# Optimization experiments

Measured on AMD Instinct MI355X. Metric: run time of the kernel, lower is better.

## Reference

```python
import jax, jax.numpy as jnp
import numpy as np

IMG_SIZE = 1280
STRIDE = 4
NUM_CLASSES = 80
TOPK = 1000
NMS_THRESH = 0.6
SCALE_CLAMP = float(np.log(1000.0))  # DEFAULT_SCALE_CLAMP
N_ANCHORS = (IMG_SIZE // STRIDE) ** 2  # 102400


def _anchors():
    # generate_anchors: meshgrid over fmp, stacked as (x, y), flattened
    fmp = IMG_SIZE // STRIDE
    ys, xs = jnp.meshgrid(jnp.arange(fmp), jnp.arange(fmp), indexing='ij')
    return jnp.stack([xs, ys], axis=-1).reshape(-1, 2).astype(jnp.float32)


def _decode_boxes(anchors, reg):
    # [wl, ht, wr, hb] -> [x1, y1, x2, y2], scaled by stride
    reg = jnp.exp(jnp.minimum(reg, SCALE_CLAMP))
    xy1 = anchors - reg[..., :2]
    xy2 = anchors + reg[..., 2:]
    return jnp.concatenate([xy1, xy2], axis=-1) * STRIDE


def _iou_matrix(b):
    # pairwise IoU with the exact eps handling of the original numpy NMS
    x1, y1, x2, y2 = b[:, 0], b[:, 1], b[:, 2], b[:, 3]
    areas = (x2 - x1) * (y2 - y1)
    xx1 = jnp.maximum(x1[:, None], x1[None, :])
    yy1 = jnp.maximum(y1[:, None], y1[None, :])
    xx2 = jnp.minimum(x2[:, None], x2[None, :])
    yy2 = jnp.minimum(y2[:, None], y2[None, :])
    w = jnp.maximum(1e-10, xx2 - xx1)
    h = jnp.maximum(1e-10, yy2 - yy1)
    inter = w * h
    return inter / (areas[:, None] + areas[None, :] - inter + 1e-10)


def _greedy_nms(iou, same_class):
    # boxes are pre-sorted by score descending (top_k output order), so a
    # single greedy pass with a same-class mask is equivalent to the
    # original per-class loop (each class subset preserves score order).
    K = iou.shape[0]
    suppress = (iou > NMS_THRESH) & same_class
    idx = jnp.arange(K)

    def body(keep, i):
        row = suppress[i] & keep[i]  # only a kept box suppresses others
        keep = keep & ~(row & (idx > i))
        return keep, None

    keep0 = jnp.ones((K,), dtype=bool)
    keep, _ = jax.lax.scan(body, keep0, idx)
    return keep


def setup_inputs() -> dict:
    key = jax.random.key(0)
    k1, k2, k3 = jax.random.split(key, 3)
    hmp_pred = jax.random.normal(k1, (N_ANCHORS, NUM_CLASSES), dtype=jnp.float32)
    reg_pred = jax.random.normal(k2, (N_ANCHORS, 4), dtype=jnp.float32)
    iou_pred = jax.random.normal(k3, (N_ANCHORS, 1), dtype=jnp.float32)
    return {"hmp_pred": hmp_pred, "reg_pred": reg_pred, "iou_pred": iou_pred}


def reference(hmp_pred, reg_pred, iou_pred):
    # score fusion: sqrt(sigmoid(hmp) * sigmoid(iou)), max over classes
    fused = jnp.sqrt(jax.nn.sigmoid(hmp_pred) * jax.nn.sigmoid(iou_pred))  # [N, C]
    scores = jnp.max(fused, axis=-1)
    labels = jnp.argmax(fused, axis=-1)

    # top-k selection (sorted descending)
    scores, indices = jax.lax.top_k(scores, TOPK)
    labels = labels[indices]
    reg = reg_pred[indices]
    anc = _anchors()[indices]

    # decode + normalize + clamp
    bboxes = jnp.clip(_decode_boxes(anc, reg) / IMG_SIZE, 0.0, 1.0)  # [K, 4]

    # class-aware greedy NMS; keep mask replaces the dynamic-shape filter
    same_class = labels[:, None] == labels[None, :]
    keep = _greedy_nms(_iou_matrix(bboxes), same_class)
    return scores, labels, bboxes, keep
```

## Files before the change

kernel.cpp:

```cpp
#include <hip/hip_runtime.h>
#include <stdint.h>

#define N_ANCH 102400
#define FMP 320
#define K_TOP 1000
#define NMS_T 0.6f
#define SC_CLAMP 6.907755278982137f
#define IMGF 1280.0f
#define NBINS 16384

#define OFF_SCORES   0u
#define OFF_LABELS   409600u
#define OFF_META     884736u
#define OFF_KEYS     884992u
#define OFF_BOXES    917760u
#define OFF_LAB1K    933760u
#define OFF_MASK     937760u
#define OFF_DIAG     1065760u

__device__ __forceinline__ float sigf(float x) {
    return 1.0f / (1.0f + expf(-x));
}

__global__ __launch_bounds__(256) void k_scores(const float* __restrict__ hmp,
                                                const float* __restrict__ iou,
                                                float* __restrict__ scores,
                                                uint32_t* __restrict__ labels,
                                                uint64_t* __restrict__ diag) {
    int blk = blockIdx.x;
    if (blk == 0) {
#pragma unroll
        for (int k = 0; k < 4; ++k) diag[threadIdx.x * 4 + k] = 0ull;
    }
    int gid = blk * 256 + threadIdx.x;
    int a = gid >> 2;
    int q = gid & 3;
    float si = sigf(iou[a]);
    const float4* row4 = (const float4*)hmp + (size_t)a * 20 + q;
    float4 v[5];
#pragma unroll
    for (int j = 0; j < 5; ++j) v[j] = row4[j * 4];
    float best = -1.0f;
    int bc = 0;
#pragma unroll
    for (int j = 0; j < 5; ++j) {
        int cb = j * 16 + q * 4;
        float f;
        f = sqrtf(sigf(v[j].x) * si); if (f > best) { best = f; bc = cb; }
        f = sqrtf(sigf(v[j].y) * si); if (f > best) { best = f; bc = cb + 1; }
        f = sqrtf(sigf(v[j].z) * si); if (f > best) { best = f; bc = cb + 2; }
        f = sqrtf(sigf(v[j].w) * si); if (f > best) { best = f; bc = cb + 3; }
    }
#pragma unroll
    for (int off = 1; off <= 2; off <<= 1) {
        float of = __shfl_xor(best, off);
        int   oc = __shfl_xor(bc, off);
        if (of > best || (of == best && oc < bc)) { best = of; bc = oc; }
    }
    if (q == 0) {
        scores[a] = best;
        labels[a] = (uint32_t)bc;
    }
}

__global__ __launch_bounds__(1024) void k_histcollect(const float* __restrict__ scores,
                                                      uint32_t* __restrict__ meta,
                                                      uint64_t* __restrict__ keys) {
    __shared__ uint32_t lh[NBINS];
    __shared__ uint32_t coarse[1024];
    __shared__ uint32_t s_cut, ccnt;

    const int tid = threadIdx.x;
    for (int i = tid; i < NBINS; i += 1024) lh[i] = 0u;
    if (tid == 0) { ccnt = 0u; s_cut = 0u; }
    __syncthreads();

    const float4* s4 = (const float4*)scores;
    for (int k = tid; k < N_ANCH / 4; k += 1024) {
        float4 v = s4[k];
        atomicAdd(&lh[__float_as_uint(v.x) >> 16], 1u);
        atomicAdd(&lh[__float_as_uint(v.y) >> 16], 1u);
        atomicAdd(&lh[__float_as_uint(v.z) >> 16], 1u);
        atomicAdd(&lh[__float_as_uint(v.w) >> 16], 1u);
    }
    __syncthreads();

    {
        uint32_t s = 0;
#pragma unroll
        for (int b = 0; b < 16; ++b) s += lh[tid * 16 + b];
        coarse[tid] = s;
    }
    __syncthreads();
    for (int off = 1; off < 1024; off <<= 1) {
        uint32_t v = coarse[tid] + ((tid + off < 1024) ? coarse[tid + off] : 0u);
        __syncthreads();
        coarse[tid] = v;
        __syncthreads();
    }
    {
        uint32_t inc   = coarse[tid];
        uint32_t above = (tid < 1023) ? coarse[tid + 1] : 0u;
        if (above < K_TOP && inc >= K_TOP) {
            uint32_t cnt = above;
            for (int b = 15; b >= 0; --b) {
                cnt += lh[tid * 16 + b];
                if (cnt >= K_TOP) { s_cut = (uint32_t)(tid * 16 + b); break; }
            }
        }
    }
    __syncthreads();

    const uint32_t cut = s_cut;
    for (int k = tid; k < N_ANCH / 4; k += 1024) {
        float4 v = s4[k];
        uint32_t bb[4] = { __float_as_uint(v.x), __float_as_uint(v.y),
                           __float_as_uint(v.z), __float_as_uint(v.w) };
#pragma unroll
        for (int c = 0; c < 4; ++c) {
            if ((bb[c] >> 16) >= cut) {
                uint32_t p = atomicAdd(&ccnt, 1u);
                if (p < 4096u)
                    keys[p] = ((uint64_t)bb[c] << 32) |
                              (uint64_t)(0xFFFFFFFFu - (uint32_t)(k * 4 + c));
            }
        }
    }
    __syncthreads();
    if (tid == 0) meta[2] = ccnt;
}

__global__ __launch_bounds__(1024) void k_rank(const uint64_t* __restrict__ keys,
                                               const uint32_t* __restrict__ meta,
                                               const uint32_t* __restrict__ labels,
                                               const float* __restrict__ reg,
                                               float* __restrict__ out,
                                               float* __restrict__ boxes,
                                               uint32_t* __restrict__ lab1k) {
    __shared__ uint64_t sk[4096];
    uint32_t M = meta[2];
    if (M > 4096u) M = 4096u;
    if ((uint32_t)(blockIdx.x * 16) >= M) return;
    for (uint32_t i = threadIdx.x; i < M; i += 1024) sk[i] = keys[i];
    __syncthreads();
    int lane = threadIdx.x & 63;
    int wg = blockIdx.x * 16 + (threadIdx.x >> 6);
    if ((uint32_t)wg >= M) return;
    uint64_t mykey = sk[wg];
    uint32_t rank = 0;
    for (uint32_t j = lane; j < M; j += 64) rank += (sk[j] > mykey) ? 1u : 0u;
#pragma unroll
    for (int off = 32; off; off >>= 1) rank += __shfl_xor(rank, off);
    if (lane != 0 || rank >= K_TOP) return;
    int t = (int)rank;
    uint32_t sbits = (uint32_t)(mykey >> 32);
    uint32_t idx   = 0xFFFFFFFFu - (uint32_t)(mykey & 0xFFFFFFFFull);
    float score = __uint_as_float(sbits);
    uint32_t lab = labels[idx];
    out[t]         = score;
    out[K_TOP + t] = (float)lab;
    lab1k[t]       = lab;
    float ax = (float)(idx % FMP);
    float ay = (float)(idx / FMP);
    float4 rr = ((const float4*)reg)[idx];
    float e0 = expf(fminf(rr.x, SC_CLAMP));
    float e1 = expf(fminf(rr.y, SC_CLAMP));
    float e2 = expf(fminf(rr.z, SC_CLAMP));
    float e3 = expf(fminf(rr.w, SC_CLAMP));
    float x1 = fminf(fmaxf((ax - e0) * 4.0f / IMGF, 0.0f), 1.0f);
    float y1 = fminf(fmaxf((ay - e1) * 4.0f / IMGF, 0.0f), 1.0f);
    float x2 = fminf(fmaxf((ax + e2) * 4.0f / IMGF, 0.0f), 1.0f);
    float y2 = fminf(fmaxf((ay + e3) * 4.0f / IMGF, 0.0f), 1.0f);
    out[2 * K_TOP + t * 4 + 0] = x1;
    out[2 * K_TOP + t * 4 + 1] = y1;
    out[2 * K_TOP + t * 4 + 2] = x2;
    out[2 * K_TOP + t * 4 + 3] = y2;
    boxes[t * 4 + 0] = x1;
    boxes[t * 4 + 1] = y1;
    boxes[t * 4 + 2] = x2;
    boxes[t * 4 + 3] = y2;
}

__global__ __launch_bounds__(1024) void k_mask(const float* __restrict__ boxes,
                                               const uint32_t* __restrict__ lab1k,
                                               uint64_t* __restrict__ mask,
                                               uint64_t* __restrict__ diag) {
    int r = blockIdx.x * 16 + (threadIdx.x >> 6);
    int lane = threadIdx.x & 63;
    if (r >= K_TOP) return;
    float4 bi = ((const float4*)boxes)[r];
    uint32_t li = lab1k[r];
    float areai = (bi.z - bi.x) * (bi.w - bi.y);
    int iw = r >> 6;
    uint64_t dw = 0ull;
#pragma unroll
    for (int w = 0; w < 16; ++w) {
        int j = w * 64 + lane;
        bool sup = false;
        if (j < K_TOP && j > r) {
            float4 bj = ((const float4*)boxes)[j];
            float areaj = (bj.z - bj.x) * (bj.w - bj.y);
            float xx1 = fmaxf(bi.x, bj.x);
            float yy1 = fmaxf(bi.y, bj.y);
            float xx2 = fminf(bi.z, bj.z);
            float yy2 = fminf(bi.w, bj.w);
            float ww = fmaxf(1e-10f, xx2 - xx1);
            float hh = fmaxf(1e-10f, yy2 - yy1);
            float inter = ww * hh;
            float iouv = inter / (areai + areaj - inter + 1e-10f);
            sup = (iouv > NMS_T) && (li == lab1k[j]);
        }
        unsigned long long m = __ballot(sup);
        if (lane == 0) mask[(size_t)r * 16 + w] = (uint64_t)m;
        if (w == iw) dw = (uint64_t)m;
    }
    if (lane == 0) diag[r] = dw;
}

__global__ __launch_bounds__(64, 1) void k_scan(const uint64_t* __restrict__ mask,
                                                const uint64_t* __restrict__ diag,
                                                float* __restrict__ out) {
    int lane = threadIdx.x;
    int q = lane >> 4, wrd = lane & 15;
    uint64_t remv = 0ull;
    uint64_t dcur = diag[lane];
    for (int g = 0; g < 16; ++g) {
        uint64_t dnxt = (g < 15) ? diag[64 * (g + 1) + lane] : 0ull;
        uint64_t bun[16];
        if (g < 15) {
#pragma unroll
            for (int r4 = 0; r4 < 16; ++r4)
                bun[r4] = mask[(size_t)(64 * g + 4 * r4 + q) * 16 + wrd];
        }
        uint32_t dlo = 0, dhi = 0;
#pragma unroll
        for (int qq = 0; qq < 4; ++qq) {
            dlo |= __builtin_amdgcn_readlane((uint32_t)remv, qq * 16 + g);
            dhi |= __builtin_amdgcn_readlane((uint32_t)(remv >> 32), qq * 16 + g);
        }
        uint64_t D = ((uint64_t)dhi << 32) | dlo;
#pragma unroll
        for (int b = 0; b < 64; ++b) {
            uint32_t tlo = __builtin_amdgcn_readlane((uint32_t)dcur, b);
            uint32_t thi = __builtin_amdgcn_readlane((uint32_t)(dcur >> 32), b);
            uint64_t T = ((uint64_t)thi << 32) | tlo;
            uint64_t sel = ((D >> b) & 1ull) - 1ull;
            D |= T & sel;
        }
        uint64_t keepg = ~D;
        int j = g * 64 + lane;
        if (j < K_TOP) out[6 * K_TOP + j] = (float)((keepg >> lane) & 1ull);
        if (g < 15) {
#pragma unroll
            for (int r4 = 0; r4 < 16; ++r4) {
                uint32_t kb = (uint32_t)(keepg >> (4 * r4 + q)) & 1u;
                uint64_t mm = 0ull - (uint64_t)kb;
                remv |= bun[r4] & mm;
            }
        }
        dcur = dnxt;
    }
}

extern "C" void kernel_launch(void* const* d_in, const int* in_sizes, int n_in,
                              void* d_out, int out_size, void* d_ws, size_t ws_size,
                              hipStream_t stream) {
    const float* hmp = (const float*)d_in[0];
    const float* reg = (const float*)d_in[1];
    const float* iou = (const float*)d_in[2];
    float* out = (float*)d_out;
    char* ws = (char*)d_ws;

    float*    scores = (float*)(ws + OFF_SCORES);
    uint32_t* labels = (uint32_t*)(ws + OFF_LABELS);
    uint32_t* meta   = (uint32_t*)(ws + OFF_META);
    uint64_t* keys   = (uint64_t*)(ws + OFF_KEYS);
    float*    boxes  = (float*)(ws + OFF_BOXES);
    uint32_t* lab1k  = (uint32_t*)(ws + OFF_LAB1K);
    uint64_t* mask   = (uint64_t*)(ws + OFF_MASK);
    uint64_t* diag   = (uint64_t*)(ws + OFF_DIAG);

    k_scores<<<dim3(N_ANCH * 4 / 256), dim3(256), 0, stream>>>(hmp, iou, scores, labels, diag);
    k_histcollect<<<dim3(1), dim3(1024), 0, stream>>>(scores, meta, keys);
    k_rank<<<dim3(256), dim3(1024), 0, stream>>>(keys, meta, labels, reg, out, boxes, lab1k);
    k_mask<<<dim3(63), dim3(1024), 0, stream>>>(boxes, lab1k, mask, diag);
    k_scan<<<dim3(1), dim3(64), 0, stream>>>(mask, diag, out);
}
```

Before: 148.6 us.

## Fuse histogram collect and rank into single kernel with bucketed rank

```diff
diff --git a/kernel.cpp b/kernel.cpp
--- a/kernel.cpp
+++ b/kernel.cpp
@@ -11,8 +11,6 @@
 
 #define OFF_SCORES   0u
 #define OFF_LABELS   409600u
-#define OFF_META     884736u
-#define OFF_KEYS     884992u
 #define OFF_BOXES    917760u
 #define OFF_LAB1K    933760u
 #define OFF_MASK     937760u
@@ -63,16 +61,24 @@
     }
 }
 
-__global__ __launch_bounds__(1024) void k_histcollect(const float* __restrict__ scores,
-                                                      uint32_t* __restrict__ meta,
-                                                      uint64_t* __restrict__ keys) {
+__global__ __launch_bounds__(1024) void k_topk(const float* __restrict__ scores,
+                                               const uint32_t* __restrict__ labels,
+                                               const float* __restrict__ reg,
+                                               float* __restrict__ out,
+                                               float* __restrict__ boxes,
+                                               uint32_t* __restrict__ lab1k) {
     __shared__ uint32_t lh[NBINS];
-    __shared__ uint32_t coarse[1024];
-    __shared__ uint32_t s_cut, ccnt;
+    __shared__ uint32_t coarse[1025];
+    __shared__ uint64_t skey[4096];
+    __shared__ uint32_t cnt[2048];
+    __shared__ uint16_t sst[4096];
+    __shared__ uint16_t sen[4096];
+    __shared__ uint32_t s_cut, s_m;
 
     const int tid = threadIdx.x;
     for (int i = tid; i < NBINS; i += 1024) lh[i] = 0u;
-    if (tid == 0) { ccnt = 0u; s_cut = 0u; }
+    for (int i = tid; i < 2048; i += 1024) cnt[i] = 0u;
+    if (tid == 0) { s_cut = 0u; coarse[1024] = 0u; }
     __syncthreads();
 
     const float4* s4 = (const float4*)scores;
@@ -102,83 +108,85 @@
         uint32_t inc   = coarse[tid];
         uint32_t above = (tid < 1023) ? coarse[tid + 1] : 0u;
         if (above < K_TOP && inc >= K_TOP) {
-            uint32_t cnt = above;
+            uint32_t c2 = above;
             for (int b = 15; b >= 0; --b) {
-                cnt += lh[tid * 16 + b];
-                if (cnt >= K_TOP) { s_cut = (uint32_t)(tid * 16 + b); break; }
+                c2 += lh[tid * 16 + b];
+                if (c2 >= K_TOP) { s_cut = (uint32_t)(tid * 16 + b); break; }
             }
         }
     }
     __syncthreads();
-
     const uint32_t cut = s_cut;
+    if (tid == 0) {
+        uint32_t tc = cut >> 4;
+        uint32_t m = coarse[tc + 1];
+        for (uint32_t k2 = cut; k2 < tc * 16 + 16; ++k2) m += lh[k2];
+        s_m = (m > 4096u) ? 4096u : m;
+    }
+
     for (int k = tid; k < N_ANCH / 4; k += 1024) {
         float4 v = s4[k];
         uint32_t bb[4] = { __float_as_uint(v.x), __float_as_uint(v.y),
                            __float_as_uint(v.z), __float_as_uint(v.w) };
 #pragma unroll
         for (int c = 0; c < 4; ++c) {
-            if ((bb[c] >> 16) >= cut) {
-                uint32_t p = atomicAdd(&ccnt, 1u);
-                if (p < 4096u)
-                    keys[p] = ((uint64_t)bb[c] << 32) |
-                              (uint64_t)(0xFFFFFFFFu - (uint32_t)(k * 4 + c));
+            uint32_t b = bb[c] >> 16;
+            if (b >= cut) {
+                uint32_t tb = b >> 4;
+                uint32_t base = coarse[tb + 1];
+                for (uint32_t k2 = b + 1; k2 < tb * 16 + 16; ++k2) base += lh[k2];
+                uint32_t sp = b - cut;
+                if (sp < 2048u) {
+                    uint32_t slot = atomicAdd(&cnt[sp], 1u);
+                    uint32_t pos  = base + slot;
+                    uint32_t end  = base + lh[b];
+                    if (pos < 4096u) {
+                        skey[pos] = ((uint64_t)bb[c] << 32) |
+                                    (uint64_t)(0xFFFFFFFFu - (uint32_t)(k * 4 + c));
+                        sst[pos] = (uint16_t)base;
+                        sen[pos] = (uint16_t)((end > 4096u) ? 4096u : end);
+                    }
+                }
             }
         }
     }
     __syncthreads();
-    if (tid == 0) meta[2] = ccnt;
-}
-
-__global__ __launch_bounds__(1024) void k_rank(const uint64_t* __restrict__ keys,
-                                               const uint32_t* __restrict__ meta,
-                                               const uint32_t* __restrict__ labels,
-                                               const float* __restrict__ reg,
-                                               float* __restrict__ out,
-                                               float* __restrict__ boxes,
-                                               uint32_t* __restrict__ lab1k) {
-    __shared__ uint64_t sk[4096];
-    uint32_t M = meta[2];
-    if (M > 4096u) M = 4096u;
-    if ((uint32_t)(blockIdx.x * 16) >= M) return;
-    for (uint32_t i = threadIdx.x; i < M; i += 1024) sk[i] = keys[i];
-    __syncthreads();
-    int lane = threadIdx.x & 63;
-    int wg = blockIdx.x * 16 + (threadIdx.x >> 6);
-    if ((uint32_t)wg >= M) return;
-    uint64_t mykey = sk[wg];
-    uint32_t rank = 0;
-    for (uint32_t j = lane; j < M; j += 64) rank += (sk[j] > mykey) ? 1u : 0u;
-#pragma unroll
-    for (int off = 32; off; off >>= 1) rank += __shfl_xor(rank, off);
-    if (lane != 0 || rank >= K_TOP) return;
-    int t = (int)rank;
-    uint32_t sbits = (uint32_t)(mykey >> 32);
-    uint32_t idx   = 0xFFFFFFFFu - (uint32_t)(mykey & 0xFFFFFFFFull);
-    float score = __uint_as_float(sbits);
-    uint32_t lab = labels[idx];
-    out[t]         = score;
-    out[K_TOP + t] = (float)lab;
-    lab1k[t]       = lab;
-    float ax = (float)(idx % FMP);
-    float ay = (float)(idx / FMP);
-    float4 rr = ((const float4*)reg)[idx];
-    float e0 = expf(fminf(rr.x, SC_CLAMP));
-    float e1 = expf(fminf(rr.y, SC_CLAMP));
-    float e2 = expf(fminf(rr.z, SC_CLAMP));
-    float e3 = expf(fminf(rr.w, SC_CLAMP));
-    float x1 = fminf(fmaxf((ax - e0) * 4.0f / IMGF, 0.0f), 1.0f);
-    float y1 = fminf(fmaxf((ay - e1) * 4.0f / IMGF, 0.0f), 1.0f);
-    float x2 = fminf(fmaxf((ax + e2) * 4.0f / IMGF, 0.0f), 1.0f);
-    float y2 = fminf(fmaxf((ay + e3) * 4.0f / IMGF, 0.0f), 1.0f);
-    out[2 * K_TOP + t * 4 + 0] = x1;
-    out[2 * K_TOP + t * 4 + 1] = y1;
-    out[2 * K_TOP + t * 4 + 2] = x2;
-    out[2 * K_TOP + t * 4 + 3] = y2;
-    boxes[t * 4 + 0] = x1;
-    boxes[t * 4 + 1] = y1;
-    boxes[t * 4 + 2] = x2;
-    boxes[t * 4 + 3] = y2;
+
+    const uint32_t M = s_m;
+    for (uint32_t s2 = tid; s2 < M; s2 += 1024) {
+        uint64_t key = skey[s2];
+        uint32_t st = sst[s2], en = sen[s2];
+        uint32_t r = st;
+        for (uint32_t u = st; u < en; ++u) r += (skey[u] > key) ? 1u : 0u;
+        if (r >= K_TOP) continue;
+        int t = (int)r;
+        uint32_t sbits = (uint32_t)(key >> 32);
+        uint32_t idx   = 0xFFFFFFFFu - (uint32_t)(key & 0xFFFFFFFFull);
+        float score = __uint_as_float(sbits);
+        uint32_t lab = labels[idx];
+        out[t]         = score;
+        out[K_TOP + t] = (float)lab;
+        lab1k[t]       = lab;
+        float ax = (float)(idx % FMP);
+        float ay = (float)(idx / FMP);
+        float4 rr = ((const float4*)reg)[idx];
+        float e0 = expf(fminf(rr.x, SC_CLAMP));
+        float e1 = expf(fminf(rr.y, SC_CLAMP));
+        float e2 = expf(fminf(rr.z, SC_CLAMP));
+        float e3 = expf(fminf(rr.w, SC_CLAMP));
+        float x1 = fminf(fmaxf((ax - e0) * 4.0f / IMGF, 0.0f), 1.0f);
+        float y1 = fminf(fmaxf((ay - e1) * 4.0f / IMGF, 0.0f), 1.0f);
+        float x2 = fminf(fmaxf((ax + e2) * 4.0f / IMGF, 0.0f), 1.0f);
+        float y2 = fminf(fmaxf((ay + e3) * 4.0f / IMGF, 0.0f), 1.0f);
+        out[2 * K_TOP + t * 4 + 0] = x1;
+        out[2 * K_TOP + t * 4 + 1] = y1;
+        out[2 * K_TOP + t * 4 + 2] = x2;
+        out[2 * K_TOP + t * 4 + 3] = y2;
+        boxes[t * 4 + 0] = x1;
+        boxes[t * 4 + 1] = y1;
+        boxes[t * 4 + 2] = x2;
+        boxes[t * 4 + 3] = y2;
+    }
 }
 
 __global__ __launch_bounds__(1024) void k_mask(const float* __restrict__ boxes,
@@ -273,16 +281,13 @@
 
     float*    scores = (float*)(ws + OFF_SCORES);
     uint32_t* labels = (uint32_t*)(ws + OFF_LABELS);
-    uint32_t* meta   = (uint32_t*)(ws + OFF_META);
-    uint64_t* keys   = (uint64_t*)(ws + OFF_KEYS);
     float*    boxes  = (float*)(ws + OFF_BOXES);
     uint32_t* lab1k  = (uint32_t*)(ws + OFF_LAB1K);
     uint64_t* mask   = (uint64_t*)(ws + OFF_MASK);
     uint64_t* diag   = (uint64_t*)(ws + OFF_DIAG);
 
     k_scores<<<dim3(N_ANCH * 4 / 256), dim3(256), 0, stream>>>(hmp, iou, scores, labels, diag);
-    k_histcollect<<<dim3(1), dim3(1024), 0, stream>>>(scores, meta, keys);
-    k_rank<<<dim3(256), dim3(1024), 0, stream>>>(keys, meta, labels, reg, out, boxes, lab1k);
+    k_topk<<<dim3(1), dim3(1024), 0, stream>>>(scores, labels, reg, out, boxes, lab1k);
     k_mask<<<dim3(63), dim3(1024), 0, stream>>>(boxes, lab1k, mask, diag);
     k_scan<<<dim3(1), dim3(64), 0, stream>>>(mask, diag, out);
 }
```

Result: slower. 178.2 us (+19.9%).

## Split single-block histogram/collect into multi-block hist and cut-collect kernels

Applied to the files above, without the earlier changes.

```diff
diff --git a/kernel.cpp b/kernel.cpp
--- a/kernel.cpp
+++ b/kernel.cpp
@@ -11,6 +11,7 @@
 
 #define OFF_SCORES   0u
 #define OFF_LABELS   409600u
+#define OFF_HIST     819200u
 #define OFF_META     884736u
 #define OFF_KEYS     884992u
 #define OFF_BOXES    917760u
@@ -26,9 +27,14 @@
                                                 const float* __restrict__ iou,
                                                 float* __restrict__ scores,
                                                 uint32_t* __restrict__ labels,
+                                                uint32_t* __restrict__ hist,
+                                                uint32_t* __restrict__ meta,
                                                 uint64_t* __restrict__ diag) {
     int blk = blockIdx.x;
-    if (blk == 0) {
+    if (blk < 64) {
+        hist[blk * 256 + threadIdx.x] = 0u;
+    } else if (blk == 64) {
+        if (threadIdx.x < 64) meta[threadIdx.x] = 0u;
 #pragma unroll
         for (int k = 0; k < 4; ++k) diag[threadIdx.x * 4 + k] = 0ull;
     }
@@ -63,26 +69,35 @@
     }
 }
 
-__global__ __launch_bounds__(1024) void k_histcollect(const float* __restrict__ scores,
-                                                      uint32_t* __restrict__ meta,
-                                                      uint64_t* __restrict__ keys) {
+__global__ __launch_bounds__(1024) void k_hist(const float* __restrict__ scores,
+                                               uint32_t* __restrict__ hist) {
+    __shared__ uint32_t lh[NBINS];
+    const int tid = threadIdx.x;
+    for (int i = tid; i < NBINS; i += 1024) lh[i] = 0u;
+    __syncthreads();
+    int base = blockIdx.x * 3200;
+    for (int k = tid; k < 3200; k += 1024) {
+        uint32_t bin = __float_as_uint(scores[base + k]) >> 16;
+        atomicAdd(&lh[bin], 1u);
+    }
+    __syncthreads();
+    for (int i = tid; i < NBINS; i += 1024) {
+        uint32_t c = lh[i];
+        if (c) atomicAdd(&hist[i], c);
+    }
+}
+
+__global__ __launch_bounds__(1024) void k_cutcollect(const float* __restrict__ scores,
+                                                     const uint32_t* __restrict__ hist,
+                                                     uint32_t* __restrict__ meta,
+                                                     uint64_t* __restrict__ keys) {
     __shared__ uint32_t lh[NBINS];
     __shared__ uint32_t coarse[1024];
-    __shared__ uint32_t s_cut, ccnt;
+    __shared__ uint32_t s_cut, cnt, cbase;
 
     const int tid = threadIdx.x;
-    for (int i = tid; i < NBINS; i += 1024) lh[i] = 0u;
-    if (tid == 0) { ccnt = 0u; s_cut = 0u; }
-    __syncthreads();
-
-    const float4* s4 = (const float4*)scores;
-    for (int k = tid; k < N_ANCH / 4; k += 1024) {
-        float4 v = s4[k];
-        atomicAdd(&lh[__float_as_uint(v.x) >> 16], 1u);
-        atomicAdd(&lh[__float_as_uint(v.y) >> 16], 1u);
-        atomicAdd(&lh[__float_as_uint(v.z) >> 16], 1u);
-        atomicAdd(&lh[__float_as_uint(v.w) >> 16], 1u);
-    }
+    for (int i = tid; i < NBINS; i += 1024) lh[i] = hist[i];
+    if (tid == 0) { s_cut = 0u; cnt = 0u; }
     __syncthreads();
 
     {
@@ -102,32 +117,37 @@
         uint32_t inc   = coarse[tid];
         uint32_t above = (tid < 1023) ? coarse[tid + 1] : 0u;
         if (above < K_TOP && inc >= K_TOP) {
-            uint32_t cnt = above;
+            uint32_t c2 = above;
             for (int b = 15; b >= 0; --b) {
-                cnt += lh[tid * 16 + b];
-                if (cnt >= K_TOP) { s_cut = (uint32_t)(tid * 16 + b); break; }
+                c2 += lh[tid * 16 + b];
+                if (c2 >= K_TOP) { s_cut = (uint32_t)(tid * 16 + b); break; }
             }
         }
     }
     __syncthreads();
 
     const uint32_t cut = s_cut;
-    for (int k = tid; k < N_ANCH / 4; k += 1024) {
-        float4 v = s4[k];
-        uint32_t bb[4] = { __float_as_uint(v.x), __float_as_uint(v.y),
-                           __float_as_uint(v.z), __float_as_uint(v.w) };
-#pragma unroll
-        for (int c = 0; c < 4; ++c) {
-            if ((bb[c] >> 16) >= cut) {
-                uint32_t p = atomicAdd(&ccnt, 1u);
-                if (p < 4096u)
-                    keys[p] = ((uint64_t)bb[c] << 32) |
-                              (uint64_t)(0xFFFFFFFFu - (uint32_t)(k * 4 + c));
-            }
-        }
-    }
-    __syncthreads();
-    if (tid == 0) meta[2] = ccnt;
+    int base = blockIdx.x * 1600;
+    uint32_t mybits[2], myi[2], mypos[2];
+    int nc = 0;
+    for (int k = tid; k < 1600; k += 1024) {
+        int i = base + k;
+        uint32_t bits = __float_as_uint(scores[i]);
+        if ((bits >> 16) >= cut) {
+            mypos[nc] = atomicAdd(&cnt, 1u);
+            mybits[nc] = bits;
+            myi[nc] = (uint32_t)i;
+            ++nc;
+        }
+    }
+    __syncthreads();
+    if (tid == 0) cbase = cnt ? atomicAdd(&meta[2], cnt) : 0u;
+    __syncthreads();
+    for (int c = 0; c < nc; ++c) {
+        uint32_t p = cbase + mypos[c];
+        if (p < 4096u)
+            keys[p] = ((uint64_t)mybits[c] << 32) | (uint64_t)(0xFFFFFFFFu - myi[c]);
+    }
 }
 
 __global__ __launch_bounds__(1024) void k_rank(const uint64_t* __restrict__ keys,
@@ -273,6 +293,7 @@
 
     float*    scores = (float*)(ws + OFF_SCORES);
     uint32_t* labels = (uint32_t*)(ws + OFF_LABELS);
+    uint32_t* hist   = (uint32_t*)(ws + OFF_HIST);
     uint32_t* meta   = (uint32_t*)(ws + OFF_META);
     uint64_t* keys   = (uint64_t*)(ws + OFF_KEYS);
     float*    boxes  = (float*)(ws + OFF_BOXES);
@@ -280,8 +301,9 @@
     uint64_t* mask   = (uint64_t*)(ws + OFF_MASK);
     uint64_t* diag   = (uint64_t*)(ws + OFF_DIAG);
 
-    k_scores<<<dim3(N_ANCH * 4 / 256), dim3(256), 0, stream>>>(hmp, iou, scores, labels, diag);
-    k_histcollect<<<dim3(1), dim3(1024), 0, stream>>>(scores, meta, keys);
+    k_scores<<<dim3(N_ANCH * 4 / 256), dim3(256), 0, stream>>>(hmp, iou, scores, labels, hist, meta, diag);
+    k_hist<<<dim3(32), dim3(1024), 0, stream>>>(scores, hist);
+    k_cutcollect<<<dim3(64), dim3(1024), 0, stream>>>(scores, hist, meta, keys);
     k_rank<<<dim3(256), dim3(1024), 0, stream>>>(keys, meta, labels, reg, out, boxes, lab1k);
     k_mask<<<dim3(63), dim3(1024), 0, stream>>>(boxes, lab1k, mask, diag);
     k_scan<<<dim3(1), dim3(64), 0, stream>>>(mask, diag, out);
```

New measurement: 135.9 us. -8.5%, faster.
